# Performance work log

Hardware: AMD Instinct MI355X
Metric: run time of the kernel (lower is better)

## Reference

```python
import jax, jax.numpy as jnp
import numpy as np

MAX_BITS = 64
HIDDEN = 256
EPS = 1e-5
TEMPERATURE = 1.0  # buffer default


def _layernorm(x, gamma, beta):
    mu = jnp.mean(x, axis=-1, keepdims=True)
    var = jnp.var(x, axis=-1, keepdims=True)
    return (x - mu) * jax.lax.rsqrt(var + EPS) * gamma + beta


def setup_inputs() -> dict:
    key = jax.random.key(0)
    ks = jax.random.split(key, 8)
    B = 32768
    # binary-ish inputs in [0,1)
    a_bits = (jax.random.uniform(ks[0], (B, MAX_BITS)) < 0.5).astype(jnp.float32)
    shift_bits = (jax.random.uniform(ks[1], (B, MAX_BITS)) < 0.5).astype(jnp.float32)
    # decoder: Linear(64,256) -> LN -> ReLU -> Linear(256,256) -> LN -> ReLU -> Linear(256,64)
    def lin(k, out_d, in_d):
        bound = 1.0 / np.sqrt(in_d)
        kw, kb = jax.random.split(k)
        W = jax.random.uniform(kw, (out_d, in_d), minval=-bound, maxval=bound)
        b = jax.random.uniform(kb, (out_d,), minval=-bound, maxval=bound)
        return W, b
    W1, b1 = lin(ks[2], HIDDEN, MAX_BITS)
    W2, b2 = lin(ks[3], HIDDEN, HIDDEN)
    W3, b3 = lin(ks[4], MAX_BITS, HIDDEN)
    g1 = jnp.ones((HIDDEN,)); be1 = jnp.zeros((HIDDEN,))
    g2 = jnp.ones((HIDDEN,)); be2 = jnp.zeros((HIDDEN,))
    return {
        "a_bits": a_bits, "shift_bits": shift_bits,
        "W1": W1, "b1": b1, "g1": g1, "be1": be1,
        "W2": W2, "b2": b2, "g2": g2, "be2": be2,
        "W3": W3, "b3": b3,
    }


def reference(a_bits, shift_bits, W1, b1, g1, be1, W2, b2, g2, be2, W3, b3):
    bits = a_bits.shape[1]
    # 2-layer MLP decoder
    h = jax.nn.relu(_layernorm(shift_bits @ W1.T + b1, g1, be1))
    h = jax.nn.relu(_layernorm(h @ W2.T + b2, g2, be2))
    shift_logits = (h @ W3.T + b3)[:, :bits]
    # training path: softmax over shift positions
    shift_probs = jax.nn.softmax(shift_logits / TEMPERATURE, axis=-1)
    # Toeplitz shift-sum: out[b,i] = sum_{s<=i} probs[b,s] * a_bits[b,i-s]
    i = jnp.arange(bits)[:, None]
    s = jnp.arange(bits)[None, :]
    idx = i - s                       # [bits, bits]
    mask = (idx >= 0)
    gath = a_bits[:, jnp.where(mask, idx, 0)] * mask.astype(a_bits.dtype)  # [B, bits, bits]
    return jnp.einsum('bis,bs->bi', gath, shift_probs)
```

## Files before the change

### kernel.cpp

```cpp
#include <hip/hip_runtime.h>
#include <hip/hip_fp16.h>


typedef short s8v __attribute__((ext_vector_type(8)));
typedef float f4v __attribute__((ext_vector_type(4)));

#define HPAD 264
#define PPAD 68

#define OFF_W1F 0
#define OFF_W2F 16384
#define OFF_W3F 81920
#define OFF_B1  98304
#define OFF_G1  98560
#define OFF_BE1 98816
#define OFF_B2  99072
#define OFF_G2  99328
#define OFF_BE2 99584
#define OFF_B3  99840

__device__ __forceinline__ float b2f(unsigned short u) {
    union { unsigned int i; float f; } v; v.i = ((unsigned int)u) << 16; return v.f;
}
__device__ __forceinline__ unsigned short f2b(float f) {
    union { float f; unsigned int i; } v; v.f = f;
    return (unsigned short)((v.i + 0x7fffu + ((v.i >> 16) & 1u)) >> 16);
}
__device__ __forceinline__ unsigned int cvtpk(float a, float b) {
    unsigned int r;
    asm("v_cvt_pk_bf16_f32 %0, %1, %2" : "=v"(r) : "v"(a), "v"(b));
    return r;
}
__device__ __forceinline__ int h2i(__half2 h) { union { __half2 h; int i; } u; u.h = h; return u.i; }
__device__ __forceinline__ __half2 i2h(int i) { union { __half2 h; int i; } u; u.i = i; return u.h; }

__device__ __forceinline__ bool probe_bf16(const void* a_bits) {
    unsigned int wv = ((const unsigned int*)a_bits)[threadIdx.x & 63];
    return __ballot((wv & 0xffffu) == 0x3f80u) != 0ULL;
}

__global__ __launch_bounds__(256) void convert_kernel(
    const void* __restrict__ a_probe,
    const void* __restrict__ W1, const void* __restrict__ W2, const void* __restrict__ W3,
    const void* __restrict__ b1, const void* __restrict__ g1, const void* __restrict__ be1,
    const void* __restrict__ b2, const void* __restrict__ g2, const void* __restrict__ be2,
    const void* __restrict__ b3,
    unsigned short* __restrict__ ws)
{
    const bool isbf = probe_bf16(a_probe);
    const int t = blockIdx.x * 256 + threadIdx.x;

    if (t < 12288) {
        const void* W; int K, idx, dstbase;
        if (t < 2048)       { idx = t;         W = W1; K = 64;  dstbase = OFF_W1F + idx * 8; }
        else if (t < 10240) { idx = t - 2048;  W = W2; K = 256; dstbase = OFF_W2F + idx * 8; }
        else                { idx = t - 10240; W = W3; K = 256; dstbase = OFF_W3F + idx * 8; }
        int nt, kc, lane;
        if (t < 2048) { nt = idx >> 7; kc = (idx >> 6) & 1; lane = idx & 63; }
        else          { nt = idx >> 9; kc = (idx >> 6) & 7; lane = idx & 63; }
        const int row = nt * 16 + (lane & 15);
        const int col = kc * 32 + (lane >> 4) * 8;
        const int src = row * K + col;
        s8v o;
        if (isbf) {
            o = *(const s8v*)((const unsigned short*)W + src);
        } else {
            const float* f = (const float*)W + src;
#pragma unroll
            for (int j = 0; j < 8; ++j) o[j] = (short)f2b(f[j]);
        }
        *(s8v*)(ws + dstbase) = o;
    } else if (t < 12488) {
        const int v = t - 12288;
        const void* srcp; int base, off;
        if (v < 32)       { srcp = b1;  base = OFF_B1;  off = v * 8; }
        else if (v < 64)  { srcp = g1;  base = OFF_G1;  off = (v - 32) * 8; }
        else if (v < 96)  { srcp = be1; base = OFF_BE1; off = (v - 64) * 8; }
        else if (v < 128) { srcp = b2;  base = OFF_B2;  off = (v - 96) * 8; }
        else if (v < 160) { srcp = g2;  base = OFF_G2;  off = (v - 128) * 8; }
        else if (v < 192) { srcp = be2; base = OFF_BE2; off = (v - 160) * 8; }
        else              { srcp = b3;  base = OFF_B3;  off = (v - 192) * 8; }
#pragma unroll
        for (int j = 0; j < 8; ++j)
            ws[base + off + j] = isbf ? ((const unsigned short*)srcp)[off + j]
                                      : f2b(((const float*)srcp)[off + j]);
    }
}

template<bool BF16>
__device__ __forceinline__ float loadS(const void* p, int idx) {
    if constexpr (BF16) return b2f(((const unsigned short*)p)[idx]);
    else return ((const float*)p)[idx];
}
template<bool BF16>
__device__ __forceinline__ s8v loadA8(const void* p, int idx) {
    if constexpr (BF16) {
        return *(const s8v*)((const unsigned short*)p + idx);
    } else {
        const float* f = (const float*)p + idx;
        f4v a = *(const f4v*)f;
        f4v b = *(const f4v*)(f + 4);
        union { s8v s; unsigned int u[4]; } r;
        r.u[0] = cvtpk(a[0], a[1]);
        r.u[1] = cvtpk(a[2], a[3]);
        r.u[2] = cvtpk(b[0], b[1]);
        r.u[3] = cvtpk(b[2], b[3]);
        return r.s;
    }
}
template<bool BF16>
__device__ __forceinline__ void storeO(void* p, int idx, float v) {
    if constexpr (BF16) ((unsigned short*)p)[idx] = f2b(v);
    else ((float*)p)[idx] = v;
}

template<bool BF16>
__device__ __forceinline__ void pipeline(
    const void* a_bits, const void* shifts, const unsigned short* ws, void* out,
    short* Hs, float* Ps, float* SS)
{
    const int tid = threadIdx.x;
    const int h = tid >> 6;
    const int l = tid & 63;
    const int q = l >> 4;
    const int c = l & 15;
    const int ntb = h << 2;
    const int grow0 = (int)blockIdx.x << 4;
    const int row = q * 4;

    f4v acc1[4];
#pragma unroll
    for (int i = 0; i < 4; ++i) acc1[i] = (f4v){0.f, 0.f, 0.f, 0.f};

    const s8v xa0 = loadA8<BF16>(shifts, (grow0 + c) * 64 + q * 8);
    const s8v xa1 = loadA8<BF16>(shifts, (grow0 + c) * 64 + 32 + q * 8);
#pragma unroll
    for (int i = 0; i < 4; ++i) {
        const int nt = ntb + i;
        s8v wb0 = *(const s8v*)(ws + OFF_W1F + ((nt * 2 + 0) * 64 + l) * 8);
        s8v wb1 = *(const s8v*)(ws + OFF_W1F + ((nt * 2 + 1) * 64 + l) * 8);
        acc1[i] = __builtin_amdgcn_mfma_f32_16x16x32_bf16(xa0, wb0, acc1[i], 0, 0, 0);
        acc1[i] = __builtin_amdgcn_mfma_f32_16x16x32_bf16(xa1, wb1, acc1[i], 0, 0, 0);
    }
    {
        float s[4] = {0, 0, 0, 0}, ss[4] = {0, 0, 0, 0};
#pragma unroll
        for (int i = 0; i < 4; ++i) {
            float bias = b2f(ws[OFF_B1 + (ntb + i) * 16 + c]);
#pragma unroll
            for (int r = 0; r < 4; ++r) {
                float v = acc1[i][r] + bias;
                acc1[i][r] = v;
                s[r] += v; ss[r] += v * v;
            }
        }
#pragma unroll
        for (int m = 1; m <= 8; m <<= 1)
#pragma unroll
            for (int r = 0; r < 4; ++r) {
                s[r]  += __shfl_xor(s[r],  m, 64);
                ss[r] += __shfl_xor(ss[r], m, 64);
            }
        if (c == 0)
#pragma unroll
            for (int r = 0; r < 4; ++r) {
                SS[(h * 16 + row + r) * 2 + 0] = s[r];
                SS[(h * 16 + row + r) * 2 + 1] = ss[r];
            }
        __syncthreads();
#pragma unroll
        for (int r = 0; r < 4; ++r) {
            float st = 0.f, sq = 0.f;
#pragma unroll
            for (int wv = 0; wv < 4; ++wv) {
                st += SS[(wv * 16 + row + r) * 2 + 0];
                sq += SS[(wv * 16 + row + r) * 2 + 1];
            }
            float mean = st * (1.0f / 256.0f);
            float var  = fmaxf(sq * (1.0f / 256.0f) - mean * mean, 0.0f);
            s[r] = mean; ss[r] = rsqrtf(var + 1e-5f);
        }
#pragma unroll
        for (int i = 0; i < 4; ++i) {
            const int nt = ntb + i;
            float gg = b2f(ws[OFF_G1 + nt * 16 + c]);
            float bb = b2f(ws[OFF_BE1 + nt * 16 + c]);
            float y[4];
#pragma unroll
            for (int r = 0; r < 4; ++r)
                y[r] = fmaxf((acc1[i][r] - s[r]) * ss[r] * gg + bb, 0.0f);
            unsigned int u01 = cvtpk(y[0], y[1]);
            unsigned int u23 = cvtpk(y[2], y[3]);
            Hs[(row + 0) * HPAD + nt * 16 + c] = (short)(u01 & 0xffffu);
            Hs[(row + 1) * HPAD + nt * 16 + c] = (short)(u01 >> 16);
            Hs[(row + 2) * HPAD + nt * 16 + c] = (short)(u23 & 0xffffu);
            Hs[(row + 3) * HPAD + nt * 16 + c] = (short)(u23 >> 16);
        }
    }
    __syncthreads();

    f4v acc2[4];
#pragma unroll
    for (int i = 0; i < 4; ++i) acc2[i] = (f4v){0.f, 0.f, 0.f, 0.f};
#pragma unroll
    for (int ks = 0; ks < 8; ++ks) {
        s8v af = *(const s8v*)&Hs[c * HPAD + ks * 32 + q * 8];
#pragma unroll
        for (int i = 0; i < 4; ++i) {
            const int nt = ntb + i;
            s8v bf_ = *(const s8v*)(ws + OFF_W2F + ((nt * 8 + ks) * 64 + l) * 8);
            acc2[i] = __builtin_amdgcn_mfma_f32_16x16x32_bf16(af, bf_, acc2[i], 0, 0, 0);
        }
    }
    {
        float s[4] = {0, 0, 0, 0}, ss[4] = {0, 0, 0, 0};
#pragma unroll
        for (int i = 0; i < 4; ++i) {
            float bias = b2f(ws[OFF_B2 + (ntb + i) * 16 + c]);
#pragma unroll
            for (int r = 0; r < 4; ++r) {
                float v = acc2[i][r] + bias;
                acc2[i][r] = v;
                s[r] += v; ss[r] += v * v;
            }
        }
#pragma unroll
        for (int m = 1; m <= 8; m <<= 1)
#pragma unroll
            for (int r = 0; r < 4; ++r) {
                s[r]  += __shfl_xor(s[r],  m, 64);
                ss[r] += __shfl_xor(ss[r], m, 64);
            }
        if (c == 0)
#pragma unroll
            for (int r = 0; r < 4; ++r) {
                SS[(h * 16 + row + r) * 2 + 0] = s[r];
                SS[(h * 16 + row + r) * 2 + 1] = ss[r];
            }
        __syncthreads();
#pragma unroll
        for (int r = 0; r < 4; ++r) {
            float st = 0.f, sq = 0.f;
#pragma unroll
            for (int wv = 0; wv < 4; ++wv) {
                st += SS[(wv * 16 + row + r) * 2 + 0];
                sq += SS[(wv * 16 + row + r) * 2 + 1];
            }
            float mean = st * (1.0f / 256.0f);
            float var  = fmaxf(sq * (1.0f / 256.0f) - mean * mean, 0.0f);
            s[r] = mean; ss[r] = rsqrtf(var + 1e-5f);
        }
#pragma unroll
        for (int i = 0; i < 4; ++i) {
            const int nt = ntb + i;
            float gg = b2f(ws[OFF_G2 + nt * 16 + c]);
            float bb = b2f(ws[OFF_BE2 + nt * 16 + c]);
            float y[4];
#pragma unroll
            for (int r = 0; r < 4; ++r)
                y[r] = fmaxf((acc2[i][r] - s[r]) * ss[r] * gg + bb, 0.0f);
            unsigned int u01 = cvtpk(y[0], y[1]);
            unsigned int u23 = cvtpk(y[2], y[3]);
            Hs[(row + 0) * HPAD + nt * 16 + c] = (short)(u01 & 0xffffu);
            Hs[(row + 1) * HPAD + nt * 16 + c] = (short)(u01 >> 16);
            Hs[(row + 2) * HPAD + nt * 16 + c] = (short)(u23 & 0xffffu);
            Hs[(row + 3) * HPAD + nt * 16 + c] = (short)(u23 >> 16);
        }
    }
    __syncthreads();

    f4v acc3 = (f4v){0.f, 0.f, 0.f, 0.f};
#pragma unroll
    for (int ks = 0; ks < 8; ++ks) {
        s8v af = *(const s8v*)&Hs[c * HPAD + ks * 32 + q * 8];
        s8v bf_ = *(const s8v*)(ws + OFF_W3F + ((h * 8 + ks) * 64 + l) * 8);
        acc3 = __builtin_amdgcn_mfma_f32_16x16x32_bf16(af, bf_, acc3, 0, 0, 0);
    }
    {
        const float bias = b2f(ws[OFF_B3 + h * 16 + c]);
        float sum[4];
#pragma unroll
        for (int r = 0; r < 4; ++r) {
            float e = __expf(acc3[r] + bias);
            Ps[(row + r) * PPAD + h * 16 + c] = e;
            sum[r] = e;
        }
#pragma unroll
        for (int m = 1; m <= 8; m <<= 1)
#pragma unroll
            for (int r = 0; r < 4; ++r)
                sum[r] += __shfl_xor(sum[r], m, 64);
        if (c == 0)
#pragma unroll
            for (int r = 0; r < 4; ++r)
                SS[(h * 16 + row + r) * 2 + 1] = sum[r];
    }
    __syncthreads();

#pragma unroll
    for (int jj = 0; jj < 2; ++jj) {
        const int j = h * 2 + jj;
        const int m0 = j, m1 = j + 8;
        float S0 = 0.f, S1 = 0.f;
#pragma unroll
        for (int wv = 0; wv < 4; ++wv) {
            S0 += SS[(wv * 16 + m0) * 2 + 1];
            S1 += SS[(wv * 16 + m1) * 2 + 1];
        }
        const float i0 = __builtin_amdgcn_rcpf(S0);
        const float i1 = __builtin_amdgcn_rcpf(S1);
        __half2 pph = __floats2half2_rn(Ps[m0 * PPAD + l] * i0,
                                        Ps[m1 * PPAD + l] * i1);
        const int ppi = h2i(pph);
        __half2 aah = __floats2half2_rn(loadS<BF16>(a_bits, (grow0 + m0) * 64 + l),
                                        loadS<BF16>(a_bits, (grow0 + m1) * 64 + l));
        int rr = h2i(aah);
        __half2 acc = __float2half2_rn(0.0f);
#pragma unroll
        for (int s = 0; s < 64; ++s) {
            const int spi = __builtin_amdgcn_readlane(ppi, s);
            acc = __hfma2(i2h(spi), i2h(rr), acc);
            if (s < 63)
                rr = __builtin_amdgcn_update_dpp(0, rr, 0x138, 0xF, 0xF, true);
        }
        storeO<BF16>(out, (grow0 + m0) * 64 + l, __low2float(acc));
        storeO<BF16>(out, (grow0 + m1) * 64 + l, __high2float(acc));
    }
}

__global__ __launch_bounds__(256, 8) void shiftdec_kernel(
    const void* __restrict__ a_bits, const void* __restrict__ shifts,
    const unsigned short* __restrict__ ws, void* __restrict__ out)
{
    __shared__ __align__(16) short Hs[16 * HPAD];
    __shared__ __align__(16) float Ps[16 * PPAD];
    __shared__ __align__(16) float SSb[4 * 16 * 2];

    if (probe_bf16(a_bits))
        pipeline<true>(a_bits, shifts, ws, out, Hs, Ps, SSb);
    else
        pipeline<false>(a_bits, shifts, ws, out, Hs, Ps, SSb);
}

extern "C" void kernel_launch(void* const* d_in, const int* in_sizes, int n_in,
                              void* d_out, int out_size, void* d_ws, size_t ws_size,
                              hipStream_t stream) {
    const int B = in_sizes[0] / 64;
    const int grid = B / 16;

    hipLaunchKernelGGL(convert_kernel, dim3(49), dim3(256), 0, stream,
                       d_in[0], d_in[2], d_in[6], d_in[10],
                       d_in[3], d_in[4], d_in[5], d_in[7], d_in[8], d_in[9], d_in[11],
                       (unsigned short*)d_ws);
    hipLaunchKernelGGL(shiftdec_kernel, dim3(grid), dim3(256), 0, stream,
                       d_in[0], d_in[1], (const unsigned short*)d_ws, d_out);
}
```

Measured before the change: 116.3 us.

## Use two waves per block, each covering twice the output columns

Halves the block size from four wavefronts to two. Each wave now computes 8 column tiles in layers 1 and 2, 2 tiles in layer 3, and 4 row pairs in the shift-sum stage. Cross-wave LayerNorm and softmax reductions now sum two partials instead of four. This gives each wave more MFMA work per shared A-fragment load and less cross-wave synchronization, at the cost of more accumulator registers and fewer waves per block to hide latency.

```diff
diff --git a/kernel.cpp b/kernel.cpp
--- a/kernel.cpp
+++ b/kernel.cpp
@@ -124,18 +124,18 @@
     const int l = tid & 63;
     const int q = l >> 4;
     const int c = l & 15;
-    const int ntb = h << 2;
+    const int ntb = h << 3;
     const int grow0 = (int)blockIdx.x << 4;
     const int row = q * 4;
 
-    f4v acc1[4];
-#pragma unroll
-    for (int i = 0; i < 4; ++i) acc1[i] = (f4v){0.f, 0.f, 0.f, 0.f};
+    f4v acc1[8];
+#pragma unroll
+    for (int i = 0; i < 8; ++i) acc1[i] = (f4v){0.f, 0.f, 0.f, 0.f};
 
     const s8v xa0 = loadA8<BF16>(shifts, (grow0 + c) * 64 + q * 8);
     const s8v xa1 = loadA8<BF16>(shifts, (grow0 + c) * 64 + 32 + q * 8);
 #pragma unroll
-    for (int i = 0; i < 4; ++i) {
+    for (int i = 0; i < 8; ++i) {
         const int nt = ntb + i;
         s8v wb0 = *(const s8v*)(ws + OFF_W1F + ((nt * 2 + 0) * 64 + l) * 8);
         s8v wb1 = *(const s8v*)(ws + OFF_W1F + ((nt * 2 + 1) * 64 + l) * 8);
@@ -145,7 +145,7 @@
     {
         float s[4] = {0, 0, 0, 0}, ss[4] = {0, 0, 0, 0};
 #pragma unroll
-        for (int i = 0; i < 4; ++i) {
+        for (int i = 0; i < 8; ++i) {
             float bias = b2f(ws[OFF_B1 + (ntb + i) * 16 + c]);
 #pragma unroll
             for (int r = 0; r < 4; ++r) {
@@ -170,18 +170,14 @@
         __syncthreads();
 #pragma unroll
         for (int r = 0; r < 4; ++r) {
-            float st = 0.f, sq = 0.f;
-#pragma unroll
-            for (int wv = 0; wv < 4; ++wv) {
-                st += SS[(wv * 16 + row + r) * 2 + 0];
-                sq += SS[(wv * 16 + row + r) * 2 + 1];
-            }
+            float st = SS[(0 * 16 + row + r) * 2 + 0] + SS[(1 * 16 + row + r) * 2 + 0];
+            float sq = SS[(0 * 16 + row + r) * 2 + 1] + SS[(1 * 16 + row + r) * 2 + 1];
             float mean = st * (1.0f / 256.0f);
             float var  = fmaxf(sq * (1.0f / 256.0f) - mean * mean, 0.0f);
             s[r] = mean; ss[r] = rsqrtf(var + 1e-5f);
         }
 #pragma unroll
-        for (int i = 0; i < 4; ++i) {
+        for (int i = 0; i < 8; ++i) {
             const int nt = ntb + i;
             float gg = b2f(ws[OFF_G1 + nt * 16 + c]);
             float bb = b2f(ws[OFF_BE1 + nt * 16 + c]);
@@ -199,14 +195,14 @@
     }
     __syncthreads();
 
-    f4v acc2[4];
-#pragma unroll
-    for (int i = 0; i < 4; ++i) acc2[i] = (f4v){0.f, 0.f, 0.f, 0.f};
+    f4v acc2[8];
+#pragma unroll
+    for (int i = 0; i < 8; ++i) acc2[i] = (f4v){0.f, 0.f, 0.f, 0.f};
 #pragma unroll
     for (int ks = 0; ks < 8; ++ks) {
         s8v af = *(const s8v*)&Hs[c * HPAD + ks * 32 + q * 8];
 #pragma unroll
-        for (int i = 0; i < 4; ++i) {
+        for (int i = 0; i < 8; ++i) {
             const int nt = ntb + i;
             s8v bf_ = *(const s8v*)(ws + OFF_W2F + ((nt * 8 + ks) * 64 + l) * 8);
             acc2[i] = __builtin_amdgcn_mfma_f32_16x16x32_bf16(af, bf_, acc2[i], 0, 0, 0);
@@ -215,7 +211,7 @@
     {
         float s[4] = {0, 0, 0, 0}, ss[4] = {0, 0, 0, 0};
 #pragma unroll
-        for (int i = 0; i < 4; ++i) {
+        for (int i = 0; i < 8; ++i) {
             float bias = b2f(ws[OFF_B2 + (ntb + i) * 16 + c]);
 #pragma unroll
             for (int r = 0; r < 4; ++r) {
@@ -240,18 +236,14 @@
         __syncthreads();
 #pragma unroll
         for (int r = 0; r < 4; ++r) {
-            float st = 0.f, sq = 0.f;
-#pragma unroll
-            for (int wv = 0; wv < 4; ++wv) {
-                st += SS[(wv * 16 + row + r) * 2 + 0];
-                sq += SS[(wv * 16 + row + r) * 2 + 1];
-            }
+            float st = SS[(0 * 16 + row + r) * 2 + 0] + SS[(1 * 16 + row + r) * 2 + 0];
+            float sq = SS[(0 * 16 + row + r) * 2 + 1] + SS[(1 * 16 + row + r) * 2 + 1];
             float mean = st * (1.0f / 256.0f);
             float var  = fmaxf(sq * (1.0f / 256.0f) - mean * mean, 0.0f);
             s[r] = mean; ss[r] = rsqrtf(var + 1e-5f);
         }
 #pragma unroll
-        for (int i = 0; i < 4; ++i) {
+        for (int i = 0; i < 8; ++i) {
             const int nt = ntb + i;
             float gg = b2f(ws[OFF_G2 + nt * 16 + c]);
             float bb = b2f(ws[OFF_BE2 + nt * 16 + c]);
@@ -269,21 +261,31 @@
     }
     __syncthreads();
 
-    f4v acc3 = (f4v){0.f, 0.f, 0.f, 0.f};
+    f4v acc3[2];
+#pragma unroll
+    for (int t = 0; t < 2; ++t) acc3[t] = (f4v){0.f, 0.f, 0.f, 0.f};
 #pragma unroll
     for (int ks = 0; ks < 8; ++ks) {
         s8v af = *(const s8v*)&Hs[c * HPAD + ks * 32 + q * 8];
-        s8v bf_ = *(const s8v*)(ws + OFF_W3F + ((h * 8 + ks) * 64 + l) * 8);
-        acc3 = __builtin_amdgcn_mfma_f32_16x16x32_bf16(af, bf_, acc3, 0, 0, 0);
+#pragma unroll
+        for (int t = 0; t < 2; ++t) {
+            const int nt = h * 2 + t;
+            s8v bf_ = *(const s8v*)(ws + OFF_W3F + ((nt * 8 + ks) * 64 + l) * 8);
+            acc3[t] = __builtin_amdgcn_mfma_f32_16x16x32_bf16(af, bf_, acc3[t], 0, 0, 0);
+        }
     }
     {
-        const float bias = b2f(ws[OFF_B3 + h * 16 + c]);
-        float sum[4];
-#pragma unroll
-        for (int r = 0; r < 4; ++r) {
-            float e = __expf(acc3[r] + bias);
-            Ps[(row + r) * PPAD + h * 16 + c] = e;
-            sum[r] = e;
+        float sum[4] = {0, 0, 0, 0};
+#pragma unroll
+        for (int t = 0; t < 2; ++t) {
+            const int nt = h * 2 + t;
+            const float bias = b2f(ws[OFF_B3 + nt * 16 + c]);
+#pragma unroll
+            for (int r = 0; r < 4; ++r) {
+                float e = __expf(acc3[t][r] + bias);
+                Ps[(row + r) * PPAD + nt * 16 + c] = e;
+                sum[r] += e;
+            }
         }
 #pragma unroll
         for (int m = 1; m <= 8; m <<= 1)
@@ -298,15 +300,11 @@
     __syncthreads();
 
 #pragma unroll
-    for (int jj = 0; jj < 2; ++jj) {
-        const int j = h * 2 + jj;
+    for (int jj = 0; jj < 4; ++jj) {
+        const int j = h * 4 + jj;
         const int m0 = j, m1 = j + 8;
-        float S0 = 0.f, S1 = 0.f;
-#pragma unroll
-        for (int wv = 0; wv < 4; ++wv) {
-            S0 += SS[(wv * 16 + m0) * 2 + 1];
-            S1 += SS[(wv * 16 + m1) * 2 + 1];
-        }
+        float S0 = SS[(0 * 16 + m0) * 2 + 1] + SS[(1 * 16 + m0) * 2 + 1];
+        float S1 = SS[(0 * 16 + m1) * 2 + 1] + SS[(1 * 16 + m1) * 2 + 1];
         const float i0 = __builtin_amdgcn_rcpf(S0);
         const float i1 = __builtin_amdgcn_rcpf(S1);
         __half2 pph = __floats2half2_rn(Ps[m0 * PPAD + l] * i0,
@@ -328,13 +326,13 @@
     }
 }
 
-__global__ __launch_bounds__(256, 8) void shiftdec_kernel(
+__global__ __launch_bounds__(128, 4) void shiftdec_kernel(
     const void* __restrict__ a_bits, const void* __restrict__ shifts,
     const unsigned short* __restrict__ ws, void* __restrict__ out)
 {
     __shared__ __align__(16) short Hs[16 * HPAD];
     __shared__ __align__(16) float Ps[16 * PPAD];
-    __shared__ __align__(16) float SSb[4 * 16 * 2];
+    __shared__ __align__(16) float SSb[2 * 16 * 2];
 
     if (probe_bf16(a_bits))
         pipeline<true>(a_bits, shifts, ws, out, Hs, Ps, SSb);
@@ -352,6 +350,6 @@
                        d_in[0], d_in[2], d_in[6], d_in[10],
                        d_in[3], d_in[4], d_in[5], d_in[7], d_in[8], d_in[9], d_in[11],
                        (unsigned short*)d_ws);
-    hipLaunchKernelGGL(shiftdec_kernel, dim3(grid), dim3(256), 0, stream,
+    hipLaunchKernelGGL(shiftdec_kernel, dim3(grid), dim3(128), 0, stream,
                        d_in[0], d_in[1], (const unsigned short*)d_ws, d_out);
 }
```

Measured after the change: 111.8 us (median of 2 runs). -3.8%, faster.
